# Kernel tuning notes

Measured on AMD Instinct MI355X. Metric: run time of the kernel, lower is better.

The kernel has to match this reference:

```python
import jax, jax.numpy as jnp
import numpy as np

IN, OUT, RANK = 4096, 4096, 256
B_SZ, SEQ = 4, 2048


def setup_inputs() -> dict:
    key = jax.random.key(0)
    ks = jax.random.split(key, 6)
    x = jax.random.normal(ks[0], (B_SZ, SEQ, IN), dtype=jnp.float32)
    base_weight = jax.random.normal(ks[1], (OUT, IN), dtype=jnp.float32) * (1.0 / np.sqrt(IN))
    A = jax.random.normal(ks[2], (RANK, IN), dtype=jnp.float32) * (1.0 / np.sqrt(IN))
    B = jax.random.normal(ks[3], (OUT, RANK), dtype=jnp.float32) * (1.0 / np.sqrt(RANK))
    d = jax.random.normal(ks[4], (RANK,), dtype=jnp.float32)
    b = jax.random.normal(ks[5], (OUT,), dtype=jnp.float32)
    return {"x": x, "base_weight": base_weight, "A": A, "B": B, "d": d, "b": b}


def reference(x, base_weight, A, B, d, b):
    # base = F.linear(x, base_weight) = x @ base_weight^T
    base = jnp.einsum('bsi,oi->bso', x, base_weight)
    # Low-rank chain: x @ (B @ (d*A))^T == ((x @ A^T) * d) @ B^T  (same math,
    # avoids materializing the full out x in vera_weight)
    xa = jnp.einsum('bsi,ri->bsr', x, A) * d  # [B,S,rank]
    adaptation = jnp.einsum('bsr,or->bso', xa, B) + b
    return base + adaptation
```

## Files before the change

### kernel.cpp

```cpp
#include <hip/hip_runtime.h>
#include <hip/hip_bf16.h>
#include <cstdint>

typedef __bf16 bf16x8 __attribute__((ext_vector_type(8)));
typedef float  f32x4  __attribute__((ext_vector_type(4)));

typedef __attribute__((address_space(3))) void lds_void;
typedef const __attribute__((address_space(1))) void gbl_cvoid;

#define GLOAD_LDS16(g, l) \
    __builtin_amdgcn_global_load_lds((gbl_cvoid*)(g), (lds_void*)(l), 16, 0, 0)

static constexpr int IN   = 4096;
static constexpr int OUT  = 4096;
static constexpr int RANK = 256;
static constexpr int M_ROWS = 4 * 2048;

__device__ __forceinline__ void cast8(const float* __restrict__ in,
                                      __bf16* __restrict__ out, int t) {
    const float4* p = (const float4*)in + (size_t)t * 2;
    float4 v0 = p[0], v1 = p[1];
    bf16x8 o;
    o[0] = (__bf16)v0.x; o[1] = (__bf16)v0.y; o[2] = (__bf16)v0.z; o[3] = (__bf16)v0.w;
    o[4] = (__bf16)v1.x; o[5] = (__bf16)v1.y; o[6] = (__bf16)v1.z; o[7] = (__bf16)v1.w;
    ((bf16x8*)out)[t] = o;
}

__global__ __launch_bounds__(256) void prep(
    const float* __restrict__ Bm, __bf16* __restrict__ Bbf,
    const float* __restrict__ A,  const float* __restrict__ d,
    __bf16* __restrict__ AdT)
{
    __shared__ float tile[64][65];
    const int blk = blockIdx.x;
    const int t   = threadIdx.x;

    if (blk < 512) {
        cast8(Bm, Bbf, blk * 256 + t);
        return;
    }
    const int ab = blk - 512;
    const int i0 = (ab & 63) * 64;
    const int r0 = (ab >> 6) * 64;
    const int cl = t & 63;
    const int rw = t >> 6;

#pragma unroll
    for (int it = 0; it < 16; ++it) {
        int rl = it * 4 + rw;
        tile[rl][cl] = A[(size_t)(r0 + rl) * IN + i0 + cl];
    }
    __syncthreads();
    float dv = d[r0 + cl];
#pragma unroll
    for (int it = 0; it < 16; ++it) {
        int il = it * 4 + rw;
        AdT[(size_t)(i0 + il) * RANK + r0 + cl] = (__bf16)(tile[cl][il] * dv);
    }
}

__global__ __launch_bounds__(256) void weff_cast(
    const __bf16* __restrict__ Bw,
    const __bf16* __restrict__ AdT,
    const float*  __restrict__ W,
    __bf16* __restrict__ Weff,
    const float*  __restrict__ x,
    __bf16* __restrict__ x_bf)
{
    __shared__ __bf16 sA[128 * 64];
    __shared__ __bf16 sB[128 * 64];

    const int blk = blockIdx.x;
    const int t   = threadIdx.x;

    if (blk >= 1024) {
        cast8(x, x_bf, (blk - 1024) * 256 + t);
        return;
    }

    constexpr int K = RANK;
    const int wave = t >> 6;
    const int lane = t & 63;
    const int quad = lane >> 4;
    const int l16  = lane & 15;
    const int m0 = (blk >> 5) * 128;
    const int n0 = (blk & 31) * 128;
    const int wm = (wave >> 1) * 64;
    const int wn = (wave & 1) * 64;
    const int xr = l16 & 7;

    f32x4 acc[4][4] = {};

    for (int kt = 0; kt < K; kt += 64) {
#pragma unroll
        for (int j = 0; j < 4; ++j) {
            int ci  = j * 256 + t;
            int row = ci >> 3;
            int kc  = (ci & 7) ^ (row & 7);
            GLOAD_LDS16(Bw  + (size_t)(m0 + row) * K + kt + kc * 8, sA + ci * 8);
        }
#pragma unroll
        for (int j = 0; j < 4; ++j) {
            int ci  = j * 256 + t;
            int row = ci >> 3;
            int kc  = (ci & 7) ^ (row & 7);
            GLOAD_LDS16(AdT + (size_t)(n0 + row) * K + kt + kc * 8, sB + ci * 8);
        }
        __syncthreads();

#pragma unroll
        for (int kk = 0; kk < 64; kk += 32) {
            const int kb = kk >> 3;
            bf16x8 a[4], b[4];
#pragma unroll
            for (int mi = 0; mi < 4; ++mi)
                a[mi] = *(const bf16x8*)(sA + (wm + mi * 16 + l16) * 64 + (((kb + quad) ^ xr) << 3));
#pragma unroll
            for (int ni = 0; ni < 4; ++ni)
                b[ni] = *(const bf16x8*)(sB + (wn + ni * 16 + l16) * 64 + (((kb + quad) ^ xr) << 3));
#pragma unroll
            for (int mi = 0; mi < 4; ++mi)
#pragma unroll
                for (int ni = 0; ni < 4; ++ni)
                    acc[mi][ni] = __builtin_amdgcn_mfma_f32_16x16x32_bf16(a[mi], b[ni], acc[mi][ni], 0, 0, 0);
        }
        __syncthreads();
    }

#pragma unroll
    for (int mi = 0; mi < 4; ++mi) {
#pragma unroll
        for (int r = 0; r < 4; ++r) {
            int row = m0 + wm + mi * 16 + quad * 4 + r;
#pragma unroll
            for (int ni = 0; ni < 4; ++ni) {
                int col = n0 + wn + ni * 16 + l16;
                size_t idx = (size_t)row * IN + col;
                Weff[idx] = (__bf16)(acc[mi][ni][r] + W[idx]);
            }
        }
    }
}


#define LD_A(BUF, mi) (*(const bf16x8*)&sX[BUF][abase + (mi) * 512])
#define LD_B(BUF, ni) (*(const bf16x8*)&sW[BUF][bbase + (ni) * 512])
#define BARR() __builtin_amdgcn_s_barrier()
#define VM(N)  asm volatile("s_waitcnt vmcnt(" #N ")")

#define STG_X(BUF, P) do { \
    GLOAD_LDS16((P),          &sX[BUF][tid * 8]); \
    GLOAD_LDS16((P) + 524288, &sX[BUF][4096 + tid * 8]); \
} while (0)
#define STG_W(BUF, P) do { \
    GLOAD_LDS16((P),          &sW[BUF][tid * 8]); \
    GLOAD_LDS16((P) + 524288, &sW[BUF][4096 + tid * 8]); \
} while (0)

#define MROW(mi, A) \
    acc[mi][0] = __builtin_amdgcn_mfma_f32_16x16x32_bf16(A, b0, acc[mi][0], 0, 0, 0); \
    acc[mi][1] = __builtin_amdgcn_mfma_f32_16x16x32_bf16(A, b1, acc[mi][1], 0, 0, 0); \
    acc[mi][2] = __builtin_amdgcn_mfma_f32_16x16x32_bf16(A, b2, acc[mi][2], 0, 0, 0); \
    acc[mi][3] = __builtin_amdgcn_mfma_f32_16x16x32_bf16(A, b3, acc[mi][3], 0, 0, 0);

#define TILE(BUF, S1, S2, VMS) \
    { \
        bf16x8 a0 = LD_A(BUF, 0), a1 = LD_A(BUF, 1), a2 = LD_A(BUF, 2), a3 = LD_A(BUF, 3); \
        b0 = LD_B(BUF, 0); b1 = LD_B(BUF, 1); b2 = LD_B(BUF, 2); b3 = LD_B(BUF, 3); \
        S1; \
        BARR(); \
        __builtin_amdgcn_s_setprio(1); \
        MROW(0, a0) MROW(1, a1) MROW(2, a2) MROW(3, a3) \
        __builtin_amdgcn_s_setprio(0); \
        BARR(); \
        a0 = LD_A(BUF, 4); a1 = LD_A(BUF, 5); a2 = LD_A(BUF, 6); a3 = LD_A(BUF, 7); \
        S2; \
        BARR(); \
        __builtin_amdgcn_s_setprio(1); \
        MROW(4, a0) MROW(5, a1) MROW(6, a2) MROW(7, a3) \
        __builtin_amdgcn_s_setprio(0); \
        VMS; \
        BARR(); \
        __builtin_amdgcn_sched_barrier(0); \
    }

__global__ __launch_bounds__(512, 2) void main_gemm(
    const __bf16* __restrict__ X,
    const __bf16* __restrict__ Wf,
    const float*  __restrict__ bias,
    float* __restrict__ out)
{
    constexpr int K = IN;
    constexpr int N = OUT;
    __shared__ __bf16 sX[4][8192];
    __shared__ __bf16 sW[4][8192];

    const int tid  = threadIdx.x;
    const int lane = tid & 63;
    const int quad = lane >> 4;
    const int l16  = lane & 15;
    const int wave = tid >> 6;
    const int wmb  = (wave >> 2) * 128;
    const int wnb  = (wave & 3) * 64;

    const int blk    = blockIdx.x;
    const int c      = blk & 7;
    const int i      = blk >> 3;
    const int n0     = (c * 2 + (i & 1)) * 256;
    const int m_base = (i >> 1) * 256;

    const int slot  = quad ^ ((l16 >> 1) & 3);
    const int abase = (wmb + l16) * 32 + slot * 8;
    const int bbase = (wnb + l16) * 32 + slot * 8;

    const int row0 = tid >> 2;
    const int ch0  = (tid & 3) ^ ((row0 >> 1) & 3);
    const __bf16* wsrc = Wf + (size_t)(n0 + row0) * K + ch0 * 8;

    float bv[4];
#pragma unroll
    for (int ni = 0; ni < 4; ++ni)
        bv[ni] = bias[n0 + wnb + ni * 16 + l16];

    bf16x8 b0, b1, b2, b3;

#pragma unroll 1
    for (int tp = 0; tp < 2; ++tp) {
        const int m0 = m_base + tp * 4096;
        const __bf16* xsrc = X + (size_t)(m0 + row0) * K + ch0 * 8;

        f32x4 acc[8][4] = {};

        STG_X(0, xsrc);      STG_W(0, wsrc);
        STG_X(1, xsrc + 32); STG_W(1, wsrc + 32);
        STG_X(2, xsrc + 64); STG_W(2, wsrc + 64);
        VM(0);
        BARR();

        const __bf16* xs = xsrc + 96;
        const __bf16* ws = wsrc + 96;

#pragma unroll 1
        for (int it = 0; it < 31; ++it) {
            TILE(0, STG_X(3, xs),      STG_W(3, ws),      VM(8))
            TILE(1, STG_X(0, xs + 32), STG_W(0, ws + 32), VM(8))
            TILE(2, STG_X(1, xs + 64), STG_W(1, ws + 64), VM(8))
            TILE(3, STG_X(2, xs + 96), STG_W(2, ws + 96), VM(8))
            xs += 128; ws += 128;
        }

        TILE(0, STG_X(3, xs), STG_W(3, ws), VM(8))
        TILE(1, (void)0,      (void)0,      VM(4))
        TILE(2, (void)0,      (void)0,      VM(0))
        TILE(3, (void)0,      (void)0,      (void)0)

#pragma unroll
        for (int mi = 0; mi < 8; ++mi) {
#pragma unroll
            for (int r = 0; r < 4; ++r) {
                int row = m0 + wmb + mi * 16 + quad * 4 + r;
#pragma unroll
                for (int ni = 0; ni < 4; ++ni) {
                    int col = n0 + wnb + ni * 16 + l16;
                    out[(size_t)row * N + col] = acc[mi][ni][r] + bv[ni];
                }
            }
        }
    }
}

#undef TILE
#undef MROW
#undef STG_X
#undef STG_W
#undef LD_A
#undef LD_B
#undef BARR
#undef VM

extern "C" void kernel_launch(void* const* d_in, const int* in_sizes, int n_in,
                              void* d_out, int out_size, void* d_ws, size_t ws_size,
                              hipStream_t stream) {
    const float* x  = (const float*)d_in[0];
    const float* W  = (const float*)d_in[1];
    const float* A  = (const float*)d_in[2];
    const float* Bm = (const float*)d_in[3];
    const float* d  = (const float*)d_in[4];
    const float* b  = (const float*)d_in[5];
    float* out = (float*)d_out;

    char* ws = (char*)d_ws;
    __bf16* x_bf   = (__bf16*)(ws);
    __bf16* weff   = (__bf16*)(ws + (size_t)67108864);
    __bf16* b_bf   = (__bf16*)(ws + (size_t)67108864 + 33554432);
    __bf16* adt_bf = (__bf16*)(ws + (size_t)67108864 + 33554432 + 2097152);

    prep<<<768, 256, 0, stream>>>(Bm, b_bf, A, d, adt_bf);
    weff_cast<<<1024 + 16384, 256, 0, stream>>>(b_bf, adt_bf, W, weff, x, x_bf);
    main_gemm<<<256, 512, 0, stream>>>(x_bf, weff, b, out);
}
```

Baseline: 532.1 us.

## Software-pipeline LDS fragment loads across K tiles with ping-pong B registers

Restructures the main GEMM inner tile so fragments for the next LDS buffer are read while MFMAs for the current tile run, using two alternating sets of B registers and split A low/high halves. Barriers per tile drop from four to one, and all global-to-LDS staging for a tile is issued in a single spot with a looser vmcnt wait. This aims to hide LDS read latency and cut synchronisation stalls in the MFMA loop. The cost is higher register pressure under launch_bounds(512,2), plus a risk of LDS read/write hazards from the reduced barriers.

```diff
diff --git a/kernel.cpp b/kernel.cpp
--- a/kernel.cpp
+++ b/kernel.cpp
@@ -157,30 +157,28 @@
     GLOAD_LDS16((P) + 524288, &sW[BUF][4096 + tid * 8]); \
 } while (0)
 
-#define MROW(mi, A) \
-    acc[mi][0] = __builtin_amdgcn_mfma_f32_16x16x32_bf16(A, b0, acc[mi][0], 0, 0, 0); \
-    acc[mi][1] = __builtin_amdgcn_mfma_f32_16x16x32_bf16(A, b1, acc[mi][1], 0, 0, 0); \
-    acc[mi][2] = __builtin_amdgcn_mfma_f32_16x16x32_bf16(A, b2, acc[mi][2], 0, 0, 0); \
-    acc[mi][3] = __builtin_amdgcn_mfma_f32_16x16x32_bf16(A, b3, acc[mi][3], 0, 0, 0);
-
-#define TILE(BUF, S1, S2, VMS) \
+#define MROW(mi, A, c0, c1, c2, c3) \
+    acc[mi][0] = __builtin_amdgcn_mfma_f32_16x16x32_bf16(A, c0, acc[mi][0], 0, 0, 0); \
+    acc[mi][1] = __builtin_amdgcn_mfma_f32_16x16x32_bf16(A, c1, acc[mi][1], 0, 0, 0); \
+    acc[mi][2] = __builtin_amdgcn_mfma_f32_16x16x32_bf16(A, c2, acc[mi][2], 0, 0, 0); \
+    acc[mi][3] = __builtin_amdgcn_mfma_f32_16x16x32_bf16(A, c3, acc[mi][3], 0, 0, 0);
+
+#define TILE_P(BUF, NBUF, c0, c1, c2, c3, n0_, n1_, n2_, n3_, STG, VMS) \
     { \
-        bf16x8 a0 = LD_A(BUF, 0), a1 = LD_A(BUF, 1), a2 = LD_A(BUF, 2), a3 = LD_A(BUF, 3); \
-        b0 = LD_B(BUF, 0); b1 = LD_B(BUF, 1); b2 = LD_B(BUF, 2); b3 = LD_B(BUF, 3); \
-        S1; \
-        BARR(); \
-        __builtin_amdgcn_s_setprio(1); \
-        MROW(0, a0) MROW(1, a1) MROW(2, a2) MROW(3, a3) \
-        __builtin_amdgcn_s_setprio(0); \
-        BARR(); \
-        a0 = LD_A(BUF, 4); a1 = LD_A(BUF, 5); a2 = LD_A(BUF, 6); a3 = LD_A(BUF, 7); \
-        S2; \
-        BARR(); \
-        __builtin_amdgcn_s_setprio(1); \
-        MROW(4, a0) MROW(5, a1) MROW(6, a2) MROW(7, a3) \
-        __builtin_amdgcn_s_setprio(0); \
         VMS; \
         BARR(); \
+        aH0 = LD_A(BUF, 4); aH1 = LD_A(BUF, 5); aH2 = LD_A(BUF, 6); aH3 = LD_A(BUF, 7); \
+        STG; \
+        __builtin_amdgcn_s_setprio(1); \
+        MROW(0, aL0, c0, c1, c2, c3) MROW(1, aL1, c0, c1, c2, c3) \
+        MROW(2, aL2, c0, c1, c2, c3) MROW(3, aL3, c0, c1, c2, c3) \
+        __builtin_amdgcn_s_setprio(0); \
+        aL0 = LD_A(NBUF, 0); aL1 = LD_A(NBUF, 1); aL2 = LD_A(NBUF, 2); aL3 = LD_A(NBUF, 3); \
+        n0_ = LD_B(NBUF, 0); n1_ = LD_B(NBUF, 1); n2_ = LD_B(NBUF, 2); n3_ = LD_B(NBUF, 3); \
+        __builtin_amdgcn_s_setprio(1); \
+        MROW(4, aH0, c0, c1, c2, c3) MROW(5, aH1, c0, c1, c2, c3) \
+        MROW(6, aH2, c0, c1, c2, c3) MROW(7, aH3, c0, c1, c2, c3) \
+        __builtin_amdgcn_s_setprio(0); \
         __builtin_amdgcn_sched_barrier(0); \
     }
 
@@ -222,37 +220,53 @@
     for (int ni = 0; ni < 4; ++ni)
         bv[ni] = bias[n0 + wnb + ni * 16 + l16];
 
-    bf16x8 b0, b1, b2, b3;
-
 #pragma unroll 1
     for (int tp = 0; tp < 2; ++tp) {
         const int m0 = m_base + tp * 4096;
         const __bf16* xsrc = X + (size_t)(m0 + row0) * K + ch0 * 8;
 
         f32x4 acc[8][4] = {};
+        bf16x8 aL0, aL1, aL2, aL3, aH0, aH1, aH2, aH3;
+        bf16x8 bx0, bx1, bx2, bx3, by0, by1, by2, by3;
 
         STG_X(0, xsrc);      STG_W(0, wsrc);
         STG_X(1, xsrc + 32); STG_W(1, wsrc + 32);
         STG_X(2, xsrc + 64); STG_W(2, wsrc + 64);
-        VM(0);
+        VM(8);
         BARR();
+        aL0 = LD_A(0, 0); aL1 = LD_A(0, 1); aL2 = LD_A(0, 2); aL3 = LD_A(0, 3);
+        bx0 = LD_B(0, 0); bx1 = LD_B(0, 1); bx2 = LD_B(0, 2); bx3 = LD_B(0, 3);
 
         const __bf16* xs = xsrc + 96;
         const __bf16* ws = wsrc + 96;
 
 #pragma unroll 1
         for (int it = 0; it < 31; ++it) {
-            TILE(0, STG_X(3, xs),      STG_W(3, ws),      VM(8))
-            TILE(1, STG_X(0, xs + 32), STG_W(0, ws + 32), VM(8))
-            TILE(2, STG_X(1, xs + 64), STG_W(1, ws + 64), VM(8))
-            TILE(3, STG_X(2, xs + 96), STG_W(2, ws + 96), VM(8))
+            TILE_P(0, 1, bx0, bx1, bx2, bx3, by0, by1, by2, by3,
+                   STG_X(3, xs); STG_W(3, ws), VM(4))
+            TILE_P(1, 2, by0, by1, by2, by3, bx0, bx1, bx2, bx3,
+                   STG_X(0, xs + 32); STG_W(0, ws + 32), VM(4))
+            TILE_P(2, 3, bx0, bx1, bx2, bx3, by0, by1, by2, by3,
+                   STG_X(1, xs + 64); STG_W(1, ws + 64), VM(4))
+            TILE_P(3, 0, by0, by1, by2, by3, bx0, bx1, bx2, bx3,
+                   STG_X(2, xs + 96); STG_W(2, ws + 96), VM(4))
             xs += 128; ws += 128;
         }
 
-        TILE(0, STG_X(3, xs), STG_W(3, ws), VM(8))
-        TILE(1, (void)0,      (void)0,      VM(4))
-        TILE(2, (void)0,      (void)0,      VM(0))
-        TILE(3, (void)0,      (void)0,      (void)0)
+        TILE_P(0, 1, bx0, bx1, bx2, bx3, by0, by1, by2, by3,
+               STG_X(3, xs); STG_W(3, ws), VM(4))
+        TILE_P(1, 2, by0, by1, by2, by3, bx0, bx1, bx2, bx3, (void)0, VM(4))
+        TILE_P(2, 3, bx0, bx1, bx2, bx3, by0, by1, by2, by3, (void)0, VM(0))
+        {
+            BARR();
+            aH0 = LD_A(3, 4); aH1 = LD_A(3, 5); aH2 = LD_A(3, 6); aH3 = LD_A(3, 7);
+            __builtin_amdgcn_s_setprio(1);
+            MROW(0, aL0, by0, by1, by2, by3) MROW(1, aL1, by0, by1, by2, by3)
+            MROW(2, aL2, by0, by1, by2, by3) MROW(3, aL3, by0, by1, by2, by3)
+            MROW(4, aH0, by0, by1, by2, by3) MROW(5, aH1, by0, by1, by2, by3)
+            MROW(6, aH2, by0, by1, by2, by3) MROW(7, aH3, by0, by1, by2, by3)
+            __builtin_amdgcn_s_setprio(0);
+        }
 
 #pragma unroll
         for (int mi = 0; mi < 8; ++mi) {
@@ -269,7 +283,7 @@
     }
 }
 
-#undef TILE
+#undef TILE_P
 #undef MROW
 #undef STG_X
 #undef STG_W
```

After: 539.1 us. About the same (+1.3%).

## Restructure GEMM pipeline into two-tile groups and split x cast kernel

Applied to the files above, without the earlier changes.

The main GEMM's LDS pipeline changes from per-tile staging with partial vmcnt waits and four barriers per tile to groups of two tiles. Each group does one full wait and barrier, then issues prefetches for the next two tiles before computing. This cuts barrier count but lowers prefetch depth to two tiles in flight and uses full waits. Separately, the x fp32-to-bf16 cast moves out of the fused weff kernel into its own grid-stride kernel with fewer blocks.

```diff
diff --git a/kernel.cpp b/kernel.cpp
--- a/kernel.cpp
+++ b/kernel.cpp
@@ -59,24 +59,24 @@
     }
 }
 
-__global__ __launch_bounds__(256) void weff_cast(
+__global__ __launch_bounds__(256) void castx(
+    const float* __restrict__ x, __bf16* __restrict__ x_bf)
+{
+    for (int i = blockIdx.x * 256 + threadIdx.x; i < 4194304; i += 2048 * 256)
+        cast8(x, x_bf, i);
+}
+
+__global__ __launch_bounds__(256) void weff(
     const __bf16* __restrict__ Bw,
     const __bf16* __restrict__ AdT,
     const float*  __restrict__ W,
-    __bf16* __restrict__ Weff,
-    const float*  __restrict__ x,
-    __bf16* __restrict__ x_bf)
+    __bf16* __restrict__ Weff)
 {
     __shared__ __bf16 sA[128 * 64];
     __shared__ __bf16 sB[128 * 64];
 
     const int blk = blockIdx.x;
     const int t   = threadIdx.x;
-
-    if (blk >= 1024) {
-        cast8(x, x_bf, (blk - 1024) * 256 + t);
-        return;
-    }
 
     constexpr int K = RANK;
     const int wave = t >> 6;
@@ -157,31 +157,35 @@
     GLOAD_LDS16((P) + 524288, &sW[BUF][4096 + tid * 8]); \
 } while (0)
 
-#define MROW(mi, A) \
-    acc[mi][0] = __builtin_amdgcn_mfma_f32_16x16x32_bf16(A, b0, acc[mi][0], 0, 0, 0); \
-    acc[mi][1] = __builtin_amdgcn_mfma_f32_16x16x32_bf16(A, b1, acc[mi][1], 0, 0, 0); \
-    acc[mi][2] = __builtin_amdgcn_mfma_f32_16x16x32_bf16(A, b2, acc[mi][2], 0, 0, 0); \
-    acc[mi][3] = __builtin_amdgcn_mfma_f32_16x16x32_bf16(A, b3, acc[mi][3], 0, 0, 0);
-
-#define TILE(BUF, S1, S2, VMS) \
+#define MROW(mi, A, c0, c1, c2, c3) \
+    acc[mi][0] = __builtin_amdgcn_mfma_f32_16x16x32_bf16(A, c0, acc[mi][0], 0, 0, 0); \
+    acc[mi][1] = __builtin_amdgcn_mfma_f32_16x16x32_bf16(A, c1, acc[mi][1], 0, 0, 0); \
+    acc[mi][2] = __builtin_amdgcn_mfma_f32_16x16x32_bf16(A, c2, acc[mi][2], 0, 0, 0); \
+    acc[mi][3] = __builtin_amdgcn_mfma_f32_16x16x32_bf16(A, c3, acc[mi][3], 0, 0, 0);
+
+#define TILE_NB(BUF) \
     { \
         bf16x8 a0 = LD_A(BUF, 0), a1 = LD_A(BUF, 1), a2 = LD_A(BUF, 2), a3 = LD_A(BUF, 3); \
-        b0 = LD_B(BUF, 0); b1 = LD_B(BUF, 1); b2 = LD_B(BUF, 2); b3 = LD_B(BUF, 3); \
-        S1; \
-        BARR(); \
+        bf16x8 c0 = LD_B(BUF, 0), c1 = LD_B(BUF, 1), c2 = LD_B(BUF, 2), c3 = LD_B(BUF, 3); \
         __builtin_amdgcn_s_setprio(1); \
-        MROW(0, a0) MROW(1, a1) MROW(2, a2) MROW(3, a3) \
+        MROW(0, a0, c0, c1, c2, c3) MROW(1, a1, c0, c1, c2, c3) \
+        MROW(2, a2, c0, c1, c2, c3) MROW(3, a3, c0, c1, c2, c3) \
         __builtin_amdgcn_s_setprio(0); \
-        BARR(); \
         a0 = LD_A(BUF, 4); a1 = LD_A(BUF, 5); a2 = LD_A(BUF, 6); a3 = LD_A(BUF, 7); \
-        S2; \
-        BARR(); \
         __builtin_amdgcn_s_setprio(1); \
-        MROW(4, a0) MROW(5, a1) MROW(6, a2) MROW(7, a3) \
+        MROW(4, a0, c0, c1, c2, c3) MROW(5, a1, c0, c1, c2, c3) \
+        MROW(6, a2, c0, c1, c2, c3) MROW(7, a3, c0, c1, c2, c3) \
         __builtin_amdgcn_s_setprio(0); \
-        VMS; \
+    }
+
+#define GRP(B0, B1, STGS) \
+    { \
+        VM(0); \
         BARR(); \
         __builtin_amdgcn_sched_barrier(0); \
+        STGS; \
+        TILE_NB(B0) \
+        TILE_NB(B1) \
     }
 
 __global__ __launch_bounds__(512, 2) void main_gemm(
@@ -222,8 +226,6 @@
     for (int ni = 0; ni < 4; ++ni)
         bv[ni] = bias[n0 + wnb + ni * 16 + l16];
 
-    bf16x8 b0, b1, b2, b3;
-
 #pragma unroll 1
     for (int tp = 0; tp < 2; ++tp) {
         const int m0 = m_base + tp * 4096;
@@ -233,26 +235,19 @@
 
         STG_X(0, xsrc);      STG_W(0, wsrc);
         STG_X(1, xsrc + 32); STG_W(1, wsrc + 32);
-        STG_X(2, xsrc + 64); STG_W(2, wsrc + 64);
-        VM(0);
-        BARR();
-
-        const __bf16* xs = xsrc + 96;
-        const __bf16* ws = wsrc + 96;
+
+        const __bf16* xs = xsrc + 64;
+        const __bf16* ws = wsrc + 64;
 
 #pragma unroll 1
         for (int it = 0; it < 31; ++it) {
-            TILE(0, STG_X(3, xs),      STG_W(3, ws),      VM(8))
-            TILE(1, STG_X(0, xs + 32), STG_W(0, ws + 32), VM(8))
-            TILE(2, STG_X(1, xs + 64), STG_W(1, ws + 64), VM(8))
-            TILE(3, STG_X(2, xs + 96), STG_W(2, ws + 96), VM(8))
+            GRP(0, 1, STG_X(2, xs); STG_W(2, ws); STG_X(3, xs + 32); STG_W(3, ws + 32))
+            GRP(2, 3, STG_X(0, xs + 64); STG_W(0, ws + 64); STG_X(1, xs + 96); STG_W(1, ws + 96))
             xs += 128; ws += 128;
         }
 
-        TILE(0, STG_X(3, xs), STG_W(3, ws), VM(8))
-        TILE(1, (void)0,      (void)0,      VM(4))
-        TILE(2, (void)0,      (void)0,      VM(0))
-        TILE(3, (void)0,      (void)0,      (void)0)
+        GRP(0, 1, STG_X(2, xs); STG_W(2, ws); STG_X(3, xs + 32); STG_W(3, ws + 32))
+        GRP(2, 3, (void)0)
 
 #pragma unroll
         for (int mi = 0; mi < 8; ++mi) {
@@ -269,7 +264,8 @@
     }
 }
 
-#undef TILE
+#undef GRP
+#undef TILE_NB
 #undef MROW
 #undef STG_X
 #undef STG_W
@@ -291,11 +287,12 @@
 
     char* ws = (char*)d_ws;
     __bf16* x_bf   = (__bf16*)(ws);
-    __bf16* weff   = (__bf16*)(ws + (size_t)67108864);
+    __bf16* weff_p = (__bf16*)(ws + (size_t)67108864);
     __bf16* b_bf   = (__bf16*)(ws + (size_t)67108864 + 33554432);
     __bf16* adt_bf = (__bf16*)(ws + (size_t)67108864 + 33554432 + 2097152);
 
     prep<<<768, 256, 0, stream>>>(Bm, b_bf, A, d, adt_bf);
-    weff_cast<<<1024 + 16384, 256, 0, stream>>>(b_bf, adt_bf, W, weff, x, x_bf);
-    main_gemm<<<256, 512, 0, stream>>>(x_bf, weff, b, out);
-}
+    weff<<<1024, 256, 0, stream>>>(b_bf, adt_bf, W, weff_p);
+    castx<<<2048, 256, 0, stream>>>(x, x_bf);
+    main_gemm<<<256, 512, 0, stream>>>(x_bf, weff_p, b, out);
+}
```

Result: slower. 586.6 us (+10.2%).
